# Performance work log

Measured on AMD Instinct MI355X. Metric: run time of the kernel, lower is better.

## Reference

```python
import jax, jax.numpy as jnp
import numpy as np

B, T, D, H = 4, 2048, 1152, 8
HD = D // H          # 144
ROT = HD             # full rotary
SCALE = HD ** -0.5


def _rotate_half(x):
    # x: [..., ROT]
    x1, x2 = x[..., : ROT // 2], x[..., ROT // 2 :]
    return jnp.concatenate([-x2, x1], axis=-1)


def _apply_rotary(q, k, cos, sin):
    # q,k: [B,H,T,HD]; cos,sin: [T,ROT] broadcast over B,H
    q_rot, q_pass = q[..., :ROT], q[..., ROT:]
    k_rot, k_pass = k[..., :ROT], k[..., ROT:]
    q = jnp.concatenate([q_rot * cos + _rotate_half(q_rot) * sin, q_pass], axis=-1)
    k = jnp.concatenate([k_rot * cos + _rotate_half(k_rot) * sin, k_pass], axis=-1)
    return q, k


def setup_inputs() -> dict:
    key = jax.random.key(0)
    ks = jax.random.split(key, 7)
    init = 1.0 / np.sqrt(D)  # keep activations well-scaled
    return {
        "x": jax.random.normal(ks[0], (B, T, D), dtype=jnp.float32),
        "cos": jax.random.uniform(ks[1], (T, ROT), dtype=jnp.float32),
        "sin": jax.random.uniform(ks[2], (T, ROT), dtype=jnp.float32),
        "Wq": jax.random.normal(ks[3], (D, D), dtype=jnp.float32) * init,
        "Wk": jax.random.normal(ks[4], (D, D), dtype=jnp.float32) * init,
        "Wv": jax.random.normal(ks[5], (D, D), dtype=jnp.float32) * init,
        "Wo": jax.random.normal(ks[6], (D, D), dtype=jnp.float32) * init,
    }


def reference(x, cos, sin, Wq, Wk, Wv, Wo):
    # nn.Linear(bias=False): y = x @ W.T
    def proj(W):
        y = jnp.einsum("btd,ed->bte", x, W)
        return y.reshape(B, T, H, HD).transpose(0, 2, 1, 3)  # [B,H,T,HD]

    q, k, v = proj(Wq), proj(Wk), proj(Wv)
    q, k = _apply_rotary(q, k, cos, sin)
    scores = jnp.einsum("bhqd,bhkd->bhqk", q, k) * SCALE
    attn = jax.nn.softmax(scores, axis=-1)
    o = jnp.einsum("bhqk,bhkd->bhqd", attn, v)
    o = o.transpose(0, 2, 1, 3).reshape(B, T, D)
    return jnp.einsum("btd,ed->bte", o, Wo)
```

## Files before the change

### kernel.cpp

```cpp
#include <hip/hip_runtime.h>
#include <cstdint>
#include <cstddef>

typedef __bf16 bf16;
typedef bf16 bf16x8 __attribute__((ext_vector_type(8)));
typedef bf16 bf16x4 __attribute__((ext_vector_type(4)));
typedef bf16 bf16x2 __attribute__((ext_vector_type(2)));
typedef float f32x4 __attribute__((ext_vector_type(4)));
typedef float f32x16 __attribute__((ext_vector_type(16)));
typedef uint32_t u32x2 __attribute__((ext_vector_type(2)));
typedef uint32_t u32x4 __attribute__((ext_vector_type(4)));

#define DEVI __device__ __forceinline__

#define CB 4
#define CT 2048
#define CD 1152
#define CH 8
#define CHD 144
#define CBT 8192

DEVI void gload_lds16(const void* g, void* l) {
  __builtin_amdgcn_global_load_lds(
      (const __attribute__((address_space(1))) void*)g,
      (__attribute__((address_space(3))) void*)l, 16, 0, 0);
}

DEVI f32x4 mfma16(bf16x8 a, bf16x8 b, f32x4 c) {
  return __builtin_amdgcn_mfma_f32_16x16x32_bf16(a, b, c, 0, 0, 0);
}
DEVI f32x16 mfma32(bf16x8 a, bf16x8 b, f32x16 c) {
  return __builtin_amdgcn_mfma_f32_32x32x16_bf16(a, b, c, 0, 0, 0);
}

DEVI uint32_t cvtpk(float lo, float hi) {
  uint32_t r;
  asm("v_cvt_pk_bf16_f32 %0, %1, %2" : "=v"(r) : "v"(lo), "v"(hi));
  return r;
}

DEVI f32x16 zero16() {
  f32x16 z;
#pragma unroll
  for (int i = 0; i < 16; ++i) z[i] = 0.f;
  return z;
}

__global__ __launch_bounds__(256) void k_cast(const float* __restrict__ in,
                                              bf16* __restrict__ out, int n8) {
  int i = blockIdx.x * 256 + threadIdx.x;
  if (i >= n8) return;
  const float4* p = (const float4*)in + (size_t)i * 2;
  float4 a = p[0], b = p[1];
  bf16x8 o;
  o[0] = (bf16)a.x; o[1] = (bf16)a.y; o[2] = (bf16)a.z; o[3] = (bf16)a.w;
  o[4] = (bf16)b.x; o[5] = (bf16)b.y; o[6] = (bf16)b.z; o[7] = (bf16)b.w;
  ((bf16x8*)out)[i] = o;
}

__global__ __launch_bounds__(256) void k_cast4(
    const float* __restrict__ a, const float* __restrict__ b,
    const float* __restrict__ c, const float* __restrict__ d,
    bf16* __restrict__ oa, bf16* __restrict__ ob,
    bf16* __restrict__ oc, bf16* __restrict__ od, int n8) {
  int w = blockIdx.y;
  const float* in = (w == 0) ? a : (w == 1) ? b : (w == 2) ? c : d;
  bf16* out = (w == 0) ? oa : (w == 1) ? ob : (w == 2) ? oc : od;
  int i = blockIdx.x * 256 + threadIdx.x;
  if (i >= n8) return;
  const float4* p = (const float4*)in + (size_t)i * 2;
  float4 x = p[0], y = p[1];
  bf16x8 o;
  o[0] = (bf16)x.x; o[1] = (bf16)x.y; o[2] = (bf16)x.z; o[3] = (bf16)x.w;
  o[4] = (bf16)y.x; o[5] = (bf16)y.y; o[6] = (bf16)y.z; o[7] = (bf16)y.w;
  ((bf16x8*)out)[i] = o;
}

template <bool BF16_OUT>
DEVI void gemm_body(const bf16* __restrict__ A, const bf16* __restrict__ W,
                    void* __restrict__ Cout, int M, int N, int K,
                    int bm0, int bn0) {
  constexpr int TBUF = 128 * 40;
  __shared__ __align__(16) bf16 As[2 * TBUF];
  __shared__ __align__(16) bf16 Bs[2 * TBUF];
  const int tid = threadIdx.x;
  const int lane = tid & 63, wid = tid >> 6;
  const int l15 = lane & 15, g = lane >> 4;
  const int wm = wid >> 1, wn = wid & 1;

  const bf16* asrc[3];
  const bf16* wsrc[3];
  int ldo[3];
  bool on[3];
#pragma unroll
  for (int c = 0; c < 3; ++c) {
    int li = tid + (c << 8);
    on[c] = (li < 640);
    int li2 = on[c] ? li : 0;
    int e0 = li2 << 3;
    int row = e0 / 40, col = e0 % 40;
    if (col >= 32) col = 24;
    asrc[c] = &A[(size_t)(bm0 + row) * K + col];
    wsrc[c] = &W[(size_t)(bn0 + row) * K + col];
    ldo[c] = (li2 & ~63) * 8;
  }

#define G_STAGE(k0, buf)                                                     \
  do {                                                                       \
    bf16* Ad = As + (buf)*TBUF;                                              \
    bf16* Bd = Bs + (buf)*TBUF;                                              \
    _Pragma("unroll") for (int c = 0; c < 3; ++c) if (on[c]) {               \
      gload_lds16(asrc[c] + (k0), Ad + ldo[c]);                              \
      gload_lds16(wsrc[c] + (k0), Bd + ldo[c]);                              \
    }                                                                        \
  } while (0)

  f32x4 acc[4][4];
  for (int mi = 0; mi < 4; ++mi)
    for (int ni = 0; ni < 4; ++ni) {
      acc[mi][ni][0] = 0.f; acc[mi][ni][1] = 0.f;
      acc[mi][ni][2] = 0.f; acc[mi][ni][3] = 0.f;
    }

  const int nk = K >> 5;
  G_STAGE(0, 0);
  __syncthreads();

  int cur = 0;
  for (int kt = 0; kt < nk; ++kt) {
    if (kt + 1 < nk) G_STAGE((kt + 1) << 5, cur ^ 1);
    __builtin_amdgcn_sched_barrier(0);

    const bf16* Ac = As + cur * TBUF;
    const bf16* Bc = Bs + cur * TBUF;
    bf16x8 af[4], bfr[4];
    for (int mi = 0; mi < 4; ++mi)
      af[mi] = *(const bf16x8*)&Ac[(wm * 64 + mi * 16 + l15) * 40 + g * 8];
    for (int ni = 0; ni < 4; ++ni)
      bfr[ni] = *(const bf16x8*)&Bc[(wn * 64 + ni * 16 + l15) * 40 + g * 8];
    __builtin_amdgcn_s_setprio(1);
    for (int mi = 0; mi < 4; ++mi)
      for (int ni = 0; ni < 4; ++ni)
        acc[mi][ni] = mfma16(af[mi], bfr[ni], acc[mi][ni]);
    __builtin_amdgcn_s_setprio(0);
    __syncthreads();
    cur ^= 1;
  }
#undef G_STAGE

  for (int mi = 0; mi < 4; ++mi)
    for (int ni = 0; ni < 4; ++ni)
      for (int r = 0; r < 4; ++r) {
        int rowg = bm0 + wm * 64 + mi * 16 + g * 4 + r;
        int colg = bn0 + wn * 64 + ni * 16 + l15;
        float v = acc[mi][ni][r];
        if (BF16_OUT)
          ((bf16*)Cout)[(size_t)rowg * N + colg] = (bf16)v;
        else
          ((float*)Cout)[(size_t)rowg * N + colg] = v;
      }
}

__global__ __launch_bounds__(256) void k_gemm_qkv(
    const bf16* __restrict__ A, const bf16* __restrict__ Wq,
    const bf16* __restrict__ Wk, const bf16* __restrict__ Wv,
    bf16* __restrict__ q, bf16* __restrict__ k, bf16* __restrict__ v) {
  const int nx = gridDim.x, ny = gridDim.y;
  const int nwg = nx * ny * gridDim.z;
  const int orig = (blockIdx.z * ny + blockIdx.y) * nx + blockIdx.x;
  const int logical = (orig & 7) * (nwg >> 3) + (orig >> 3);
  const int lx = logical % nx;
  const int rest = logical / nx;
  const int ly = rest % ny, lz = rest / ny;
  const bf16* W = (lz == 0) ? Wq : (lz == 1) ? Wk : Wv;
  bf16* out = (lz == 0) ? q : (lz == 1) ? k : v;
  gemm_body<true>(A, W, out, CBT, CD, CD, ly * 128, lx * 128);
}

__global__ __launch_bounds__(256) void k_gemm_out(
    const bf16* __restrict__ A, const bf16* __restrict__ W, float* __restrict__ out) {
  const int nx = gridDim.x, ny = gridDim.y;
  const int nwg = nx * ny;
  const int orig = blockIdx.y * nx + blockIdx.x;
  const int logical = (orig & 7) * (nwg >> 3) + (orig >> 3);
  const int lx = logical % nx, ly = logical / nx;
  gemm_body<false>(A, W, out, CBT, CD, CD, ly * 128, lx * 128);
}

__global__ __launch_bounds__(256) void k_rotary(bf16* __restrict__ q, bf16* __restrict__ k,
                                                const float* __restrict__ cosb,
                                                const float* __restrict__ sinb) {
  const int bt = blockIdx.x;
  const int t = bt & (CT - 1);
  const size_t rowoff = (size_t)bt * CD;
  const float* cr = cosb + (size_t)t * CHD;
  const float* sr = sinb + (size_t)t * CHD;
  for (int i = threadIdx.x; i < 288; i += 256) {
    int tensor = i / 144;
    int rem = i - tensor * 144;
    int h = rem / 18, jg = rem % 18;
    int j = jg * 4;
    float scl = tensor ? 1.0f : 0.120224587f;
    bf16* base = (tensor ? k : q) + rowoff + h * CHD;
    bf16x4 a = *(bf16x4*)&base[j];
    bf16x4 b2 = *(bf16x4*)&base[j + 72];
    f32x4 c1 = *(const f32x4*)&cr[j];
    f32x4 s1 = *(const f32x4*)&sr[j];
    f32x4 c2 = *(const f32x4*)&cr[j + 72];
    f32x4 s2 = *(const f32x4*)&sr[j + 72];
    bf16x4 o1, o2;
    for (int r = 0; r < 4; ++r) {
      float av = (float)a[r], bv = (float)b2[r];
      o1[r] = (bf16)((av * c1[r] - bv * s1[r]) * scl);
      o2[r] = (bf16)((bv * c2[r] + av * s2[r]) * scl);
    }
    *(bf16x4*)&base[j] = o1;
    *(bf16x4*)&base[j + 72] = o2;
  }
}

__global__ __launch_bounds__(256) void k_vtrans(const bf16* __restrict__ v, bf16* __restrict__ vT) {
  __shared__ bf16 tile[64][152];
  const int bh = blockIdx.y;
  const int b = bh >> 3, h = bh & 7;
  const int t0 = blockIdx.x * 64;
  for (int i8 = threadIdx.x; i8 < 64 * 18; i8 += 256) {
    int r = i8 / 18, c8 = i8 % 18;
    *(bf16x8*)&tile[r][c8 * 8] =
        *(const bf16x8*)&v[((size_t)(b * CT + t0 + r)) * CD + h * CHD + c8 * 8];
  }
  __syncthreads();
  for (int o = threadIdx.x; o < CHD * 64; o += 256) {
    int hd = o / 64, j = o & 63;
    vT[((size_t)(bh * CHD + hd)) * CT + t0 + j] = tile[j][hd];
  }
}

DEVI void build_pfrag(const f32x16& s, float m, float& ps, bf16x8& f0, bf16x8& f1) {
  uint32_t pk[8];
#pragma unroll
  for (int a = 0; a < 8; ++a) {
    float p0 = exp2f(s[2 * a] - m);
    float p1 = exp2f(s[2 * a + 1] - m);
    ps += p0 + p1;
    pk[a] = cvtpk(p0, p1);
  }
  u32x2 r02 = __builtin_amdgcn_permlane32_swap(pk[0], pk[2], false, false);
  u32x2 r13 = __builtin_amdgcn_permlane32_swap(pk[1], pk[3], false, false);
  u32x2 r46 = __builtin_amdgcn_permlane32_swap(pk[4], pk[6], false, false);
  u32x2 r57 = __builtin_amdgcn_permlane32_swap(pk[5], pk[7], false, false);
  u32x4 w0 = {r02[0], r13[0], r02[1], r13[1]};
  u32x4 w1 = {r46[0], r57[0], r46[1], r57[1]};
  f0 = __builtin_bit_cast(bf16x8, w0);
  f1 = __builtin_bit_cast(bf16x8, w1);
}

DEVI float max32(const f32x16& s0, const f32x16& s1) {
  float q0 = fmaxf(fmaxf(s0[0], s0[1]), fmaxf(s0[2], s0[3]));
  float q1 = fmaxf(fmaxf(s0[4], s0[5]), fmaxf(s0[6], s0[7]));
  float q2 = fmaxf(fmaxf(s0[8], s0[9]), fmaxf(s0[10], s0[11]));
  float q3 = fmaxf(fmaxf(s0[12], s0[13]), fmaxf(s0[14], s0[15]));
  float q4 = fmaxf(fmaxf(s1[0], s1[1]), fmaxf(s1[2], s1[3]));
  float q5 = fmaxf(fmaxf(s1[4], s1[5]), fmaxf(s1[6], s1[7]));
  float q6 = fmaxf(fmaxf(s1[8], s1[9]), fmaxf(s1[10], s1[11]));
  float q7 = fmaxf(fmaxf(s1[12], s1[13]), fmaxf(s1[14], s1[15]));
  return fmaxf(fmaxf(fmaxf(q0, q1), fmaxf(q2, q3)),
               fmaxf(fmaxf(q4, q5), fmaxf(q6, q7)));
}

__global__ __launch_bounds__(256, 2) void k_attn(const bf16* __restrict__ qg,
                                                 const bf16* __restrict__ kg,
                                                 const bf16* __restrict__ vT,
                                                 bf16* __restrict__ og) {
  const int lin = blockIdx.x;
  const int xcd = lin & 7, idx = lin >> 3;
  const int bh = ((idx & 3) << 3) | xcd;
  const int qx = idx >> 2;
  const int b = bh >> 3, h = bh & 7;
  const int q0 = qx << 7;
  const int tid = threadIdx.x, lane = tid & 63, wq = tid >> 6;
  const int l31 = lane & 31, hi = lane >> 5;
  const int hi16 = hi * 16;
  const int kx7 = l31 & 7;
  const int kxor = kx7 << 4;

  constexpr int KBUF = 64 * 144;
  constexpr int VBUF = 160 * 64;
  __shared__ __align__(16) bf16 Ks[2 * KBUF];
  __shared__ __align__(16) bf16 Vs[2 * VBUF];

  bf16x8 qf[9];
  {
    const bf16* qbase = qg + (size_t)(b * CT + q0 + wq * 32 + l31) * CD + h * CHD + hi * 8;
#pragma unroll
    for (int ks = 0; ks < 9; ++ks) qf[ks] = *(const bf16x8*)&qbase[ks * 16];
  }

  const bf16* ksrc[5];
  const bf16* vsrc[5];
  int kldo[5], vldo[5];
#pragma unroll
  for (int it = 0; it < 5; ++it) {
    int c = tid + it * 256;
    if (c >= 1152) c = 0;
    int krow = c / 18, kj = c - krow * 18;
    int kgr = (kj < 16) ? (kj ^ (krow & 7)) : kj;
    ksrc[it] = kg + (size_t)(b * CT + krow) * CD + h * CHD + kgr * 8;
    kldo[it] = (c & ~63) * 8;
    int vr = c >> 3, vj = c & 7;
    int vgr = vj ^ (vr & 7);
    vsrc[it] = vT + (size_t)(bh * CHD + vr) * CT + vgr * 8;
    vldo[it] = (c & ~63) * 8;
  }

  {
    u32x4 z = {0u, 0u, 0u, 0u};
    int bsel = tid >> 7, off = tid & 127;
    *(u32x4*)(Vs + bsel * VBUF + 144 * 64 + off * 8) = z;
  }

#define STAGE_TILE(kv, buf)                                                 \
  do {                                                                      \
    bf16* Kn = Ks + (buf)*KBUF;                                             \
    bf16* Vn = Vs + (buf)*VBUF;                                             \
    _Pragma("unroll") for (int it = 0; it < 4; ++it) {                      \
      gload_lds16(ksrc[it] + (size_t)(kv)*CD, Kn + kldo[it]);               \
      gload_lds16(vsrc[it] + (kv), Vn + vldo[it]);                          \
    }                                                                       \
    if (tid < 128) {                                                        \
      gload_lds16(ksrc[4] + (size_t)(kv)*CD, Kn + kldo[4]);                 \
      gload_lds16(vsrc[4] + (kv), Vn + vldo[4]);                            \
    }                                                                       \
  } while (0)

  STAGE_TILE(0, 0);
  __syncthreads();

  f32x16 oacc[5];
#pragma unroll
  for (int u = 0; u < 5; ++u) oacc[u] = zero16();
  float mrow = -__builtin_inff();
  float lsum = 0.f;

  int cur = 0;
  for (int t = 0; t < 32; ++t) {
    bf16* Kc = Ks + cur * KBUF;
    bf16* Vc = Vs + cur * VBUF;

    if (t < 31) STAGE_TILE((t + 1) << 6, cur ^ 1);
    __builtin_amdgcn_sched_barrier(0);

    const char* kr0 = (const char*)Kc + (size_t)l31 * 288;
    const char* kr1 = kr0 + 32 * 288;
    f32x16 s0 = zero16(), s1 = zero16();
    __builtin_amdgcn_s_setprio(1);
#pragma unroll
    for (int ks = 0; ks < 9; ++ks) {
      int cc = 2 * ks + hi;
      int off = ((ks < 8) ? (cc ^ kx7) : cc) << 4;
      s0 = mfma32(*(const bf16x8*)(kr0 + off), qf[ks], s0);
      s1 = mfma32(*(const bf16x8*)(kr1 + off), qf[ks], s1);
    }
    __builtin_amdgcn_s_setprio(0);

    float mt = max32(s0, s1);
    mt = fmaxf(mt, __shfl_xor(mt, 32));

    if (mt > mrow + 8.0f) {
      float alpha = exp2f(mrow - mt);
      lsum *= alpha;
#pragma unroll
      for (int u = 0; u < 5; ++u) oacc[u] = oacc[u] * alpha;
      mrow = mt;
    }

    float ps = 0.f;
    bf16x8 pf0, pf1, pf2, pf3;
    build_pfrag(s0, mrow, ps, pf0, pf1);
    build_pfrag(s1, mrow, ps, pf2, pf3);
    ps += __shfl_xor(ps, 32);
    lsum += ps;

    __builtin_amdgcn_s_setprio(1);
#pragma unroll
    for (int u = 0; u < 5; ++u) {
      const char* vrow = (const char*)Vc + (size_t)(u * 32 + l31) * 128;
      oacc[u] = mfma32(*(const bf16x8*)(vrow + ((0 * 32 + hi16) ^ kxor)), pf0, oacc[u]);
      oacc[u] = mfma32(*(const bf16x8*)(vrow + ((1 * 32 + hi16) ^ kxor)), pf1, oacc[u]);
      oacc[u] = mfma32(*(const bf16x8*)(vrow + ((2 * 32 + hi16) ^ kxor)), pf2, oacc[u]);
      oacc[u] = mfma32(*(const bf16x8*)(vrow + ((3 * 32 + hi16) ^ kxor)), pf3, oacc[u]);
    }
    __builtin_amdgcn_s_setprio(0);

    __syncthreads();
    cur ^= 1;
  }
#undef STAGE_TILE

  float inv = 1.0f / lsum;
  bf16* ob = og + (size_t)(b * CT + q0 + wq * 32 + l31) * CD + h * CHD;
#pragma unroll
  for (int u = 0; u < 5; ++u) {
#pragma unroll
    for (int pr = 0; pr < 8; ++pr) {
      if (u == 4 && pr >= 4) continue;
      int hd = u * 32 + ((2 * pr) & 3) + 8 * (pr >> 1) + 4 * hi;
      bf16x2 w;
      w[0] = (bf16)(oacc[u][2 * pr] * inv);
      w[1] = (bf16)(oacc[u][2 * pr + 1] * inv);
      *(bf16x2*)&ob[hd] = w;
    }
  }
}

extern "C" void kernel_launch(void* const* d_in, const int* in_sizes, int n_in,
                              void* d_out, int out_size, void* d_ws, size_t ws_size,
                              hipStream_t stream) {
  const float* x = (const float*)d_in[0];
  const float* cosb = (const float*)d_in[1];
  const float* sinb = (const float*)d_in[2];
  const float* Wq = (const float*)d_in[3];
  const float* Wk = (const float*)d_in[4];
  const float* Wv = (const float*)d_in[5];
  const float* Wo = (const float*)d_in[6];

  char* ws = (char*)d_ws;
  bf16* xb   = (bf16*)(ws + 0);
  bf16* wqb  = (bf16*)(ws + 18874368);
  bf16* wkb  = (bf16*)(ws + 21528576);
  bf16* wvb  = (bf16*)(ws + 24182784);
  bf16* wob  = (bf16*)(ws + 26836992);
  bf16* qlin = (bf16*)(ws + 29491200);
  bf16* klin = (bf16*)(ws + 48365568);
  bf16* vlin = (bf16*)(ws + 67239936);
  bf16* vT   = (bf16*)(ws + 86114304);

  k_cast<<<4608, 256, 0, stream>>>(x, xb, CBT * CD / 8);
  k_cast4<<<dim3(648, 4), 256, 0, stream>>>(Wq, Wk, Wv, Wo, wqb, wkb, wvb, wob,
                                            CD * CD / 8);

  k_gemm_qkv<<<dim3(CD / 128, CBT / 128, 3), 256, 0, stream>>>(xb, wqb, wkb, wvb,
                                                               qlin, klin, vlin);
  k_rotary<<<CB * CT, 256, 0, stream>>>(qlin, klin, cosb, sinb);
  k_vtrans<<<dim3(CT / 64, CB * CH), 256, 0, stream>>>(vlin, vT);
  k_attn<<<512, 256, 0, stream>>>(qlin, klin, vT, xb);
  k_gemm_out<<<dim3(CD / 128, CBT / 128), 256, 0, stream>>>(xb, wob, (float*)d_out);
}
```

Before: 253.2 us.

## Fuse rotary and V transpose into QKV GEMM epilogue, fold row-sum into PV MFMA

The Wq/Wk rows are permuted during the weight cast so rotate-half pairs land in adjacent columns. The QKV GEMM epilogue then applies rotary via a lane shuffle, and the V projection writes directly in transposed layout. This drops the separate rotary and V-transpose kernels and the extra round trip of q/k/v through global memory. In attention, a row of ones in the padded V tile makes the PV MFMA produce the softmax denominator, removing the per-tile scalar sum and shuffle. The cost is scattered cos/sin loads and transposed 8-byte stores in the GEMM epilogue.

```diff
diff --git a/kernel.cpp b/kernel.cpp
--- a/kernel.cpp
+++ b/kernel.cpp
@@ -73,13 +73,21 @@
   bf16x8 o;
   o[0] = (bf16)x.x; o[1] = (bf16)x.y; o[2] = (bf16)x.z; o[3] = (bf16)x.w;
   o[4] = (bf16)y.x; o[5] = (bf16)y.y; o[6] = (bf16)y.z; o[7] = (bf16)y.w;
-  ((bf16x8*)out)[i] = o;
-}
-
-template <bool BF16_OUT>
+  int oi = i;
+  if (w < 2) {
+    int e = i / 144, ch = i - e * 144;
+    int h2 = e / CHD, j = e - h2 * CHD;
+    int ep = h2 * CHD + ((j < 72) ? (2 * j) : (2 * (j - 72) + 1));
+    oi = ep * 144 + ch;
+  }
+  ((bf16x8*)out)[oi] = o;
+}
+
+template <int MODE>
 DEVI void gemm_body(const bf16* __restrict__ A, const bf16* __restrict__ W,
-                    void* __restrict__ Cout, int M, int N, int K,
-                    int bm0, int bn0) {
+                    void* __restrict__ Cout, int bm0, int bn0, float scl,
+                    const float* __restrict__ cosb, const float* __restrict__ sinb) {
+  constexpr int K = CD, N = CD;
   constexpr int TBUF = 128 * 40;
   __shared__ __align__(16) bf16 As[2 * TBUF];
   __shared__ __align__(16) bf16 Bs[2 * TBUF];
@@ -148,23 +156,54 @@
   }
 #undef G_STAGE
 
-  for (int mi = 0; mi < 4; ++mi)
-    for (int ni = 0; ni < 4; ++ni)
-      for (int r = 0; r < 4; ++r) {
-        int rowg = bm0 + wm * 64 + mi * 16 + g * 4 + r;
-        int colg = bn0 + wn * 64 + ni * 16 + l15;
-        float v = acc[mi][ni][r];
-        if (BF16_OUT)
-          ((bf16*)Cout)[(size_t)rowg * N + colg] = (bf16)v;
-        else
-          ((float*)Cout)[(size_t)rowg * N + colg] = v;
+  if (MODE == 0) {
+    for (int ni = 0; ni < 4; ++ni) {
+      int colg = bn0 + wn * 64 + ni * 16 + l15;
+      int s = colg % CHD;
+      int p = s >> 1;
+      bool even = !(colg & 1);
+      int cidx = even ? p : (72 + p);
+      for (int mi = 0; mi < 4; ++mi)
+        for (int r = 0; r < 4; ++r) {
+          int rowg = bm0 + wm * 64 + mi * 16 + g * 4 + r;
+          int tloc = rowg & (CT - 1);
+          float cv = cosb[(size_t)tloc * CHD + cidx];
+          float sv = sinb[(size_t)tloc * CHD + cidx];
+          float own = acc[mi][ni][r];
+          float oth = __shfl_xor(own, 1);
+          float o = even ? (own * cv - oth * sv) : (own * cv + oth * sv);
+          ((bf16*)Cout)[(size_t)rowg * N + colg] = (bf16)(o * scl);
+        }
+    }
+  } else if (MODE == 1) {
+    for (int ni = 0; ni < 4; ++ni) {
+      int colg = bn0 + wn * 64 + ni * 16 + l15;
+      int h2 = colg / CHD, hd = colg - h2 * CHD;
+      for (int mi = 0; mi < 4; ++mi) {
+        int rowg0 = bm0 + wm * 64 + mi * 16 + g * 4;
+        int b2 = rowg0 >> 11;
+        int t = rowg0 & (CT - 1);
+        bf16x4 w4;
+        for (int r = 0; r < 4; ++r) w4[r] = (bf16)acc[mi][ni][r];
+        *(bf16x4*)&((bf16*)Cout)[((size_t)((b2 * CH + h2) * CHD + hd)) * CT + t] = w4;
       }
+    }
+  } else {
+    for (int mi = 0; mi < 4; ++mi)
+      for (int ni = 0; ni < 4; ++ni)
+        for (int r = 0; r < 4; ++r) {
+          int rowg = bm0 + wm * 64 + mi * 16 + g * 4 + r;
+          int colg = bn0 + wn * 64 + ni * 16 + l15;
+          ((float*)Cout)[(size_t)rowg * N + colg] = acc[mi][ni][r];
+        }
+  }
 }
 
 __global__ __launch_bounds__(256) void k_gemm_qkv(
     const bf16* __restrict__ A, const bf16* __restrict__ Wq,
     const bf16* __restrict__ Wk, const bf16* __restrict__ Wv,
-    bf16* __restrict__ q, bf16* __restrict__ k, bf16* __restrict__ v) {
+    bf16* __restrict__ q, bf16* __restrict__ k, bf16* __restrict__ vT,
+    const float* __restrict__ cosb, const float* __restrict__ sinb) {
   const int nx = gridDim.x, ny = gridDim.y;
   const int nwg = nx * ny * gridDim.z;
   const int orig = (blockIdx.z * ny + blockIdx.y) * nx + blockIdx.x;
@@ -172,9 +211,12 @@
   const int lx = logical % nx;
   const int rest = logical / nx;
   const int ly = rest % ny, lz = rest / ny;
-  const bf16* W = (lz == 0) ? Wq : (lz == 1) ? Wk : Wv;
-  bf16* out = (lz == 0) ? q : (lz == 1) ? k : v;
-  gemm_body<true>(A, W, out, CBT, CD, CD, ly * 128, lx * 128);
+  if (lz == 0)
+    gemm_body<0>(A, Wq, q, ly * 128, lx * 128, 0.120224587f, cosb, sinb);
+  else if (lz == 1)
+    gemm_body<0>(A, Wk, k, ly * 128, lx * 128, 1.0f, cosb, sinb);
+  else
+    gemm_body<1>(A, Wv, vT, ly * 128, lx * 128, 0.f, cosb, sinb);
 }
 
 __global__ __launch_bounds__(256) void k_gemm_out(
@@ -184,65 +226,15 @@
   const int orig = blockIdx.y * nx + blockIdx.x;
   const int logical = (orig & 7) * (nwg >> 3) + (orig >> 3);
   const int lx = logical % nx, ly = logical / nx;
-  gemm_body<false>(A, W, out, CBT, CD, CD, ly * 128, lx * 128);
-}
-
-__global__ __launch_bounds__(256) void k_rotary(bf16* __restrict__ q, bf16* __restrict__ k,
-                                                const float* __restrict__ cosb,
-                                                const float* __restrict__ sinb) {
-  const int bt = blockIdx.x;
-  const int t = bt & (CT - 1);
-  const size_t rowoff = (size_t)bt * CD;
-  const float* cr = cosb + (size_t)t * CHD;
-  const float* sr = sinb + (size_t)t * CHD;
-  for (int i = threadIdx.x; i < 288; i += 256) {
-    int tensor = i / 144;
-    int rem = i - tensor * 144;
-    int h = rem / 18, jg = rem % 18;
-    int j = jg * 4;
-    float scl = tensor ? 1.0f : 0.120224587f;
-    bf16* base = (tensor ? k : q) + rowoff + h * CHD;
-    bf16x4 a = *(bf16x4*)&base[j];
-    bf16x4 b2 = *(bf16x4*)&base[j + 72];
-    f32x4 c1 = *(const f32x4*)&cr[j];
-    f32x4 s1 = *(const f32x4*)&sr[j];
-    f32x4 c2 = *(const f32x4*)&cr[j + 72];
-    f32x4 s2 = *(const f32x4*)&sr[j + 72];
-    bf16x4 o1, o2;
-    for (int r = 0; r < 4; ++r) {
-      float av = (float)a[r], bv = (float)b2[r];
-      o1[r] = (bf16)((av * c1[r] - bv * s1[r]) * scl);
-      o2[r] = (bf16)((bv * c2[r] + av * s2[r]) * scl);
-    }
-    *(bf16x4*)&base[j] = o1;
-    *(bf16x4*)&base[j + 72] = o2;
-  }
-}
-
-__global__ __launch_bounds__(256) void k_vtrans(const bf16* __restrict__ v, bf16* __restrict__ vT) {
-  __shared__ bf16 tile[64][152];
-  const int bh = blockIdx.y;
-  const int b = bh >> 3, h = bh & 7;
-  const int t0 = blockIdx.x * 64;
-  for (int i8 = threadIdx.x; i8 < 64 * 18; i8 += 256) {
-    int r = i8 / 18, c8 = i8 % 18;
-    *(bf16x8*)&tile[r][c8 * 8] =
-        *(const bf16x8*)&v[((size_t)(b * CT + t0 + r)) * CD + h * CHD + c8 * 8];
-  }
-  __syncthreads();
-  for (int o = threadIdx.x; o < CHD * 64; o += 256) {
-    int hd = o / 64, j = o & 63;
-    vT[((size_t)(bh * CHD + hd)) * CT + t0 + j] = tile[j][hd];
-  }
-}
-
-DEVI void build_pfrag(const f32x16& s, float m, float& ps, bf16x8& f0, bf16x8& f1) {
+  gemm_body<2>(A, W, out, ly * 128, lx * 128, 0.f, nullptr, nullptr);
+}
+
+DEVI void build_pfrag(const f32x16& s, float m, bf16x8& f0, bf16x8& f1) {
   uint32_t pk[8];
 #pragma unroll
   for (int a = 0; a < 8; ++a) {
     float p0 = exp2f(s[2 * a] - m);
     float p1 = exp2f(s[2 * a + 1] - m);
-    ps += p0 + p1;
     pk[a] = cvtpk(p0, p1);
   }
   u32x2 r02 = __builtin_amdgcn_permlane32_swap(pk[0], pk[2], false, false);
@@ -314,9 +306,13 @@
   }
 
   {
-    u32x4 z = {0u, 0u, 0u, 0u};
     int bsel = tid >> 7, off = tid & 127;
-    *(u32x4*)(Vs + bsel * VBUF + 144 * 64 + off * 8) = z;
+    int row = 144 + (off >> 3), cj = off & 7;
+    uint32_t one2 = 0x3F803F80u;
+    u32x4 val;
+    if (row == 144) { val[0] = one2; val[1] = one2; val[2] = one2; val[3] = one2; }
+    else { val[0] = 0u; val[1] = 0u; val[2] = 0u; val[3] = 0u; }
+    *(u32x4*)(Vs + bsel * VBUF + row * 64 + cj * 8) = val;
   }
 
 #define STAGE_TILE(kv, buf)                                                 \
@@ -340,7 +336,6 @@
 #pragma unroll
   for (int u = 0; u < 5; ++u) oacc[u] = zero16();
   float mrow = -__builtin_inff();
-  float lsum = 0.f;
 
   int cur = 0;
   for (int t = 0; t < 32; ++t) {
@@ -368,18 +363,14 @@
 
     if (mt > mrow + 8.0f) {
       float alpha = exp2f(mrow - mt);
-      lsum *= alpha;
 #pragma unroll
       for (int u = 0; u < 5; ++u) oacc[u] = oacc[u] * alpha;
       mrow = mt;
     }
 
-    float ps = 0.f;
     bf16x8 pf0, pf1, pf2, pf3;
-    build_pfrag(s0, mrow, ps, pf0, pf1);
-    build_pfrag(s1, mrow, ps, pf2, pf3);
-    ps += __shfl_xor(ps, 32);
-    lsum += ps;
+    build_pfrag(s0, mrow, pf0, pf1);
+    build_pfrag(s1, mrow, pf2, pf3);
 
     __builtin_amdgcn_s_setprio(1);
 #pragma unroll
@@ -397,7 +388,11 @@
   }
 #undef STAGE_TILE
 
-  float inv = 1.0f / lsum;
+  float ls = oacc[4][8];
+  float lo = __shfl_xor(ls, 32);
+  if (hi) ls = lo;
+  float inv = 1.0f / ls;
+
   bf16* ob = og + (size_t)(b * CT + q0 + wq * 32 + l31) * CD + h * CHD;
 #pragma unroll
   for (int u = 0; u < 5; ++u) {
@@ -432,17 +427,14 @@
   bf16* wob  = (bf16*)(ws + 26836992);
   bf16* qlin = (bf16*)(ws + 29491200);
   bf16* klin = (bf16*)(ws + 48365568);
-  bf16* vlin = (bf16*)(ws + 67239936);
-  bf16* vT   = (bf16*)(ws + 86114304);
+  bf16* vT   = (bf16*)(ws + 67239936);
 
   k_cast<<<4608, 256, 0, stream>>>(x, xb, CBT * CD / 8);
   k_cast4<<<dim3(648, 4), 256, 0, stream>>>(Wq, Wk, Wv, Wo, wqb, wkb, wvb, wob,
                                             CD * CD / 8);
 
-  k_gemm_qkv<<<dim3(CD / 128, CBT / 128, 3), 256, 0, stream>>>(xb, wqb, wkb, wvb,
-                                                               qlin, klin, vlin);
-  k_rotary<<<CB * CT, 256, 0, stream>>>(qlin, klin, cosb, sinb);
-  k_vtrans<<<dim3(CT / 64, CB * CH), 256, 0, stream>>>(vlin, vT);
+  k_gemm_qkv<<<dim3(CD / 128, CBT / 128, 3), 256, 0, stream>>>(
+      xb, wqb, wkb, wvb, qlin, klin, vT, cosb, sinb);
   k_attn<<<512, 256, 0, stream>>>(qlin, klin, vT, xb);
   k_gemm_out<<<dim3(CD / 128, CBT / 128), 256, 0, stream>>>(xb, wob, (float*)d_out);
 }
```

Measured after the change: 275.9 us. +9.0%, slower.
